# Performance work log

Measured on AMD Instinct MI355X. Metric: run time of the kernel, lower is better.

## Reference

```python
import jax, jax.numpy as jnp
import numpy as np

REP_DIM = 256
ATT_DIM = 256
AGRU_DIM = 256
BATCH = 64
MAX_FACTS = 512


def setup_inputs() -> dict:
    key = jax.random.key(0)
    ks = jax.random.split(key, 16)

    def lin(k, out_d, in_d):
        return jax.random.normal(k, (out_d, in_d), dtype=jnp.float32) / np.sqrt(in_d)

    inp = {
        "queries": jax.random.normal(ks[0], (BATCH, 1, REP_DIM), dtype=jnp.float32),
        "facts": jax.random.normal(ks[1], (BATCH, MAX_FACTS, REP_DIM), dtype=jnp.float32),
        "num_facts": jax.random.randint(ks[2], (BATCH,), 1, MAX_FACTS + 1, dtype=jnp.int32),
        "m_old": jax.random.normal(ks[3], (BATCH, 1, REP_DIM), dtype=jnp.float32),
        # attention MLP
        "W1_w": lin(ks[4], ATT_DIM, 4 * REP_DIM),
        "W1_b": jnp.zeros((ATT_DIM,), jnp.float32),
        "W2_w": lin(ks[5], 1, ATT_DIM),
        "W2_b": jnp.zeros((1,), jnp.float32),
        # attention GRU cell
        "Wr_w": lin(ks[6], AGRU_DIM, REP_DIM),
        "Ur_w": lin(ks[7], AGRU_DIM, AGRU_DIM),
        "Ur_b": jnp.zeros((AGRU_DIM,), jnp.float32),
        "Wg_w": lin(ks[8], AGRU_DIM, REP_DIM),
        "Ug_w": lin(ks[9], AGRU_DIM, AGRU_DIM),
        "Ug_b": jnp.zeros((AGRU_DIM,), jnp.float32),
        # output transform
        "Wt_w": lin(ks[10], REP_DIM, 2 * REP_DIM + AGRU_DIM),
        "Wt_b": jnp.zeros((REP_DIM,), jnp.float32),
    }
    return inp


def _forward(queries, facts, num_facts, m_old,
             W1_w, W1_b, W2_w, W2_b,
             Wr_w, Ur_w, Ur_b, Wg_w, Ug_w, Ug_b,
             Wt_w, Wt_b):
    B, T, D = facts.shape

    # ---- attention scores ----
    q = queries  # (B,1,D) broadcasts
    m = m_old
    z = jnp.concatenate(
        [facts * q, facts * m, jnp.abs(facts - q), jnp.abs(facts - m)], axis=2
    )  # (B,T,4D)
    Z = jnp.tanh(jnp.einsum("btf,af->bta", z, W1_w) + W1_b)
    Z = jnp.einsum("bta,oa->bto", Z, W2_w) + W2_b  # (B,T,1)
    mask = (jnp.arange(T)[None, :] < num_facts[:, None])[..., None]  # (B,T,1)
    Z = jnp.where(mask, Z, -jnp.inf)
    g = jax.nn.softmax(Z, axis=1)  # (B,T,1)

    # ---- attention GRU (sequential scan over facts) ----
    h0 = m_old[:, 0]  # (B,A)

    def step(h, xs):
        fact, g_t = xs  # (B,D), (B,1)
        r = jax.nn.sigmoid(fact @ Wr_w.T + h @ Ur_w.T + Ur_b)
        h_t = jnp.tanh(fact @ Wg_w.T + r * (h @ Ug_w.T + Ug_b))
        h_new = g_t * h_t + (1.0 - g_t) * h
        return h_new, h_new

    xs = (jnp.swapaxes(facts, 0, 1), jnp.swapaxes(g, 0, 1))  # (T,B,D),(T,B,1)
    _, states = jax.lax.scan(step, h0, xs)  # (T,B,A)
    c = jnp.take_along_axis(
        states, (num_facts - 1)[None, :, None].astype(jnp.int32), axis=0
    )[0]  # (B,A)

    # ---- next memory ----
    cat = jnp.concatenate([m_old[:, 0], c, queries[:, 0]], axis=1)
    m_new = jax.nn.relu(cat @ Wt_w.T + Wt_b)
    return m_new[:, None, :]  # (B,1,D)


def reference(queries, facts, num_facts, m_old,
              W1_w, W1_b, W2_w, W2_b,
              Wr_w, Ur_w, Ur_b, Wg_w, Ug_w, Ug_b,
              Wt_w, Wt_b):
    return _forward(queries, facts, num_facts, m_old,
                    W1_w, W1_b, W2_w, W2_b,
                    Wr_w, Ur_w, Ur_b, Wg_w, Ug_w, Ug_b,
                    Wt_w, Wt_b)
```

## Files before the change

### kernel.cpp

```cpp
#include <hip/hip_runtime.h>
#include <hip/hip_fp16.h>
#include <stdint.h>

#define B 64
#define T 512
#define D 256

typedef _Float16 f16;
typedef __attribute__((ext_vector_type(8))) _Float16 f16x8;
typedef __attribute__((ext_vector_type(4))) _Float16 f16x4;
typedef __attribute__((ext_vector_type(2))) _Float16 f16x2;
typedef __attribute__((ext_vector_type(4))) float f32x4;
typedef __attribute__((ext_vector_type(4))) unsigned int u32x4;

static __device__ __forceinline__ float dot2f(f16x2 a, f16x2 b, float c) {
  return __builtin_amdgcn_fdot2(a, b, c, false);
}
static __device__ __forceinline__ f16x2 as_h2(unsigned int u) {
  return __builtin_bit_cast(f16x2, u);
}

__global__ void k_convert(const float* __restrict__ W1, const float* __restrict__ Wr,
                          const float* __restrict__ Wg,
                          f16* __restrict__ W1h, f16* __restrict__ Wrh, f16* __restrict__ Wgh)
{
  const int64_t n1 = 256 * 1024, n2 = 65536, n3 = 65536;
  int64_t stride = (int64_t)gridDim.x * blockDim.x;
  for (int64_t i = (int64_t)blockIdx.x * blockDim.x + threadIdx.x; i < n1 + n2 + n3; i += stride) {
    if (i < n1)           W1h[i] = (f16)W1[i];
    else if (i < n1 + n2) Wrh[i - n1] = (f16)Wr[i - n1];
    else                  Wgh[i - n1 - n2] = (f16)Wg[i - n1 - n2];
  }
}

__global__ __launch_bounds__(256, 2) void k_attn(
    const float* __restrict__ facts, const float* __restrict__ queries,
    const float* __restrict__ m_old, const f16* __restrict__ W1h,
    const float* __restrict__ W1_b, const float* __restrict__ W2_w,
    const float* __restrict__ W2_b, float* __restrict__ Zlog)
{
  const int b = blockIdx.y;
  const int t0 = blockIdx.x * 32;
  const int tid = threadIdx.x;
  const int lane = tid & 63;
  const int wave = tid >> 6;
  const int lr = lane & 15;
  const int lg = lane >> 4;

  __shared__ float q_s[D], m_s[D];
  __shared__ __align__(16) char zbuf[32 * 2048];
  __shared__ float part[4][32];

  q_s[tid] = queries[b * D + tid];
  m_s[tid] = m_old[b * D + tid];
  __syncthreads();

  for (int e = tid; e < 32 * 128; e += 256) {
    int t = e >> 7;
    int j2 = e & 127;
    int j = j2 * 2;
    const float2 f2 = *(const float2*)(facts + ((int64_t)(b * T) + t0 + t) * D + j);
    float q0 = q_s[j], q1 = q_s[j + 1], mm0 = m_s[j], mm1 = m_s[j + 1];
    f16x2 z0; z0[0] = (f16)(f2.x * q0);        z0[1] = (f16)(f2.y * q1);
    f16x2 z1; z1[0] = (f16)(f2.x * mm0);       z1[1] = (f16)(f2.y * mm1);
    f16x2 z2; z2[0] = (f16)fabsf(f2.x - q0);   z2[1] = (f16)fabsf(f2.y - q1);
    f16x2 z3; z3[0] = (f16)fabsf(f2.x - mm0);  z3[1] = (f16)fabsf(f2.y - mm1);
    int xr = (t & 7) << 4;
    int base = t * 2048;
    *(f16x2*)(zbuf + ((base + (0 * 128 + j2) * 4) ^ xr)) = z0;
    *(f16x2*)(zbuf + ((base + (1 * 128 + j2) * 4) ^ xr)) = z1;
    *(f16x2*)(zbuf + ((base + (2 * 128 + j2) * 4) ^ xr)) = z2;
    *(f16x2*)(zbuf + ((base + (3 * 128 + j2) * 4) ^ xr)) = z3;
  }
  __syncthreads();

  const int n0 = wave * 64;
  f32x4 acc[2][4];
  #pragma unroll
  for (int i = 0; i < 2; ++i)
    #pragma unroll
    for (int j = 0; j < 4; ++j) acc[i][j] = (f32x4){0.f, 0.f, 0.f, 0.f};

  #pragma unroll 2
  for (int ks = 0; ks < 32; ++ks) {
    f16x8 af[2];
    #pragma unroll
    for (int mt = 0; mt < 2; ++mt) {
      int row = mt * 16 + lr;
      int byte = (row * 2048 + ks * 64 + lg * 16) ^ ((row & 7) << 4);
      af[mt] = *(const f16x8*)(zbuf + byte);
    }
    #pragma unroll
    for (int nt = 0; nt < 4; ++nt) {
      int a = n0 + nt * 16 + lr;
      f16x8 bf = *(const f16x8*)(W1h + (int64_t)a * 1024 + ks * 32 + lg * 8);
      acc[0][nt] = __builtin_amdgcn_mfma_f32_16x16x32_f16(af[0], bf, acc[0][nt], 0, 0, 0);
      acc[1][nt] = __builtin_amdgcn_mfma_f32_16x16x32_f16(af[1], bf, acc[1][nt], 0, 0, 0);
    }
  }

  float pr[2][4] = {{0.f, 0.f, 0.f, 0.f}, {0.f, 0.f, 0.f, 0.f}};
  #pragma unroll
  for (int nt = 0; nt < 4; ++nt) {
    int a = n0 + nt * 16 + lr;
    float b1 = W1_b[a];
    float w2 = W2_w[a];
    #pragma unroll
    for (int mt = 0; mt < 2; ++mt)
      #pragma unroll
      for (int r = 0; r < 4; ++r)
        pr[mt][r] += tanhf(acc[mt][nt][r] + b1) * w2;
  }
  #pragma unroll
  for (int mt = 0; mt < 2; ++mt)
    #pragma unroll
    for (int r = 0; r < 4; ++r) {
      float v = pr[mt][r];
      v += __shfl_xor(v, 1, 64);
      v += __shfl_xor(v, 2, 64);
      v += __shfl_xor(v, 4, 64);
      v += __shfl_xor(v, 8, 64);
      pr[mt][r] = v;
    }
  if ((lane & 15) == 0) {
    #pragma unroll
    for (int mt = 0; mt < 2; ++mt)
      #pragma unroll
      for (int r = 0; r < 4; ++r)
        part[wave][mt * 16 + lg * 4 + r] = pr[mt][r];
  }
  __syncthreads();
  if (tid < 32)
    Zlog[b * T + t0 + tid] = part[0][tid] + part[1][tid] + part[2][tid] + part[3][tid] + W2_b[0];
}

__global__ __launch_bounds__(256, 2) void k_factproj(
    const float* __restrict__ facts, const f16* __restrict__ Wrh, const f16* __restrict__ Wgh,
    const float* __restrict__ Ur_b, f16* __restrict__ Frh, f16* __restrict__ Fgh)
{
  const int b = blockIdx.y;
  const int t0 = blockIdx.x * 64;
  const int tid = threadIdx.x;
  const int lane = tid & 63;
  const int wave = tid >> 6;
  const int lr = lane & 15;
  const int lg = lane >> 4;

  __shared__ __align__(16) char albuf[64 * 512];

  for (int c = tid; c < 64 * 32; c += 256) {
    int row = c >> 5;
    int kc = c & 31;
    const float* src = facts + ((int64_t)(b * T) + t0 + row) * D + kc * 8;
    float4 x0 = *(const float4*)src;
    float4 x1 = *(const float4*)(src + 4);
    f16x8 v;
    v[0] = (f16)x0.x; v[1] = (f16)x0.y; v[2] = (f16)x0.z; v[3] = (f16)x0.w;
    v[4] = (f16)x1.x; v[5] = (f16)x1.y; v[6] = (f16)x1.z; v[7] = (f16)x1.w;
    int byte = (row * 512 + kc * 16) ^ ((row & 7) << 4);
    *(f16x8*)(albuf + byte) = v;
  }
  __syncthreads();

  f32x4 accr[16], accg[16];
  #pragma unroll
  for (int i = 0; i < 16; ++i) { accr[i] = (f32x4){0.f,0.f,0.f,0.f}; accg[i] = (f32x4){0.f,0.f,0.f,0.f}; }

  const int arow = wave * 16 + lr;
  #pragma unroll 2
  for (int ks = 0; ks < 8; ++ks) {
    int byte = (arow * 512 + ks * 64 + lg * 16) ^ ((arow & 7) << 4);
    f16x8 af = *(const f16x8*)(albuf + byte);
    #pragma unroll
    for (int nt = 0; nt < 16; ++nt) {
      int a = nt * 16 + lr;
      f16x8 br = *(const f16x8*)(Wrh + a * 256 + ks * 32 + lg * 8);
      f16x8 bg = *(const f16x8*)(Wgh + a * 256 + ks * 32 + lg * 8);
      accr[nt] = __builtin_amdgcn_mfma_f32_16x16x32_f16(af, br, accr[nt], 0, 0, 0);
      accg[nt] = __builtin_amdgcn_mfma_f32_16x16x32_f16(af, bg, accg[nt], 0, 0, 0);
    }
  }

  #pragma unroll
  for (int nt = 0; nt < 16; ++nt) {
    int col = nt * 16 + lr;
    float urb = Ur_b[col];
    #pragma unroll
    for (int r = 0; r < 4; ++r) {
      int t = t0 + wave * 16 + lg * 4 + r;
      int64_t off = ((int64_t)(b * T) + t) * D + col;
      Frh[off] = (f16)(accr[nt][r] + urb);
      Fgh[off] = (f16)(accg[nt][r]);
    }
  }
}

__global__ __launch_bounds__(256, 1) void k_scan_v6(
    const float* __restrict__ Zlog, const int* __restrict__ num_facts,
    const f16* __restrict__ Frh, const f16* __restrict__ Fgh,
    const float* __restrict__ Ur_w, const float* __restrict__ Ug_w,
    const float* __restrict__ Ug_b, const float* __restrict__ m_old,
    const float* __restrict__ queries, const float* __restrict__ Wt_w,
    const float* __restrict__ Wt_b, float* __restrict__ out)
{
  const int b = blockIdx.x;
  const int tid = threadIdx.x;
  const int lane = tid & 63;
  const int w = tid >> 6;
  const int q = lane >> 5;
  const int p = w * 32 + (lane & 31);
  const int nf = num_facts[b];

  __shared__ __align__(16) char hbuf[2][544];
  __shared__ float g_lds[512];
  __shared__ float redM[4], redS[4];
  __shared__ __align__(16) float cat_s[768];

  {
    float z0 = Zlog[b * 512 + tid];
    float z1 = Zlog[b * 512 + 256 + tid];
    float v0 = (tid < nf) ? z0 : -INFINITY;
    float v1 = (tid + 256 < nf) ? z1 : -INFINITY;
    float mx = fmaxf(v0, v1);
    #pragma unroll
    for (int s = 1; s < 64; s <<= 1) mx = fmaxf(mx, __shfl_xor(mx, s, 64));
    if (lane == 0) redM[w] = mx;
    __syncthreads();
    mx = fmaxf(fmaxf(redM[0], redM[1]), fmaxf(redM[2], redM[3]));
    float e0 = (tid < nf) ? __expf(v0 - mx) : 0.f;
    float e1 = (tid + 256 < nf) ? __expf(v1 - mx) : 0.f;
    float sum = e0 + e1;
    #pragma unroll
    for (int s = 1; s < 64; s <<= 1) sum += __shfl_xor(sum, s, 64);
    if (lane == 0) redS[w] = sum;
    __syncthreads();
    float inv = 1.f / (redS[0] + redS[1] + redS[2] + redS[3]);
    g_lds[tid] = e0 * inv;
    g_lds[256 + tid] = e1 * inv;
  }

  f16x2 wR[2][64], wG[2][64];
  #pragma unroll
  for (int j = 0; j < 2; ++j) {
    const float* ur = Ur_w + (int64_t)(2 * p + j) * 256 + q * 128;
    const float* ug = Ug_w + (int64_t)(2 * p + j) * 256 + q * 128;
    #pragma unroll
    for (int c = 0; c < 32; ++c) {
      float4 a = *(const float4*)(ur + c * 4);
      float4 g4 = *(const float4*)(ug + c * 4);
      f16x2 p0; p0[0] = (f16)a.x;  p0[1] = (f16)a.y;
      f16x2 p1; p1[0] = (f16)a.z;  p1[1] = (f16)a.w;
      f16x2 q0; q0[0] = (f16)g4.x; q0[1] = (f16)g4.y;
      f16x2 q1; q1[0] = (f16)g4.z; q1[1] = (f16)g4.w;
      wR[j][c * 2 + 0] = p0;
      wR[j][c * 2 + 1] = p1;
      wG[j][c * 2 + 0] = q0;
      wG[j][c * 2 + 1] = q1;
    }
  }

  float2 h2 = *(const float2*)(m_old + (int64_t)b * 256 + 2 * p);
  float h0 = h2.x, h1 = h2.y;
  float2 ub2 = *(const float2*)(Ug_b + 2 * p);

  const int waddr = 4 * p + (p >= 64 ? 16 : 0);
  if (q == 0) {
    f16x2 hp; hp[0] = (f16)h0; hp[1] = (f16)h1;
    *(f16x2*)(&hbuf[0][waddr]) = hp;
  }

  const f16* __restrict__ frp = Frh + (int64_t)(b * T) * D + 2 * p;
  const f16* __restrict__ fgp = Fgh + (int64_t)(b * T) * D + 2 * p;
  f16x2 frv = *(const f16x2*)frp;
  f16x2 fgv = *(const f16x2*)fgp;

  __syncthreads();

  for (int t = 0; t < nf; ++t) {
    const char* hb = hbuf[t & 1] + q * 272;
    u32x4 hv[4];
    #pragma unroll
    for (int c = 0; c < 4; ++c) hv[c] = *(const u32x4*)(hb + c * 16);
    u32x4 hw[4];
    #pragma unroll
    for (int c = 0; c < 4; ++c) hw[c] = *(const u32x4*)(hb + 64 + c * 16);
    u32x4 hx[4];
    #pragma unroll
    for (int c = 0; c < 4; ++c) hx[c] = *(const u32x4*)(hb + 128 + c * 16);
    u32x4 hy[4];
    #pragma unroll
    for (int c = 0; c < 4; ++c) hy[c] = *(const u32x4*)(hb + 192 + c * 16);

    f16x2 nfr = {}, nfg = {};
    if (t + 1 < nf) {
      nfr = *(const f16x2*)(frp + (int64_t)(t + 1) * D);
      nfg = *(const f16x2*)(fgp + (int64_t)(t + 1) * D);
    }
    float gt = g_lds[t];

    float aR0a = 0.f, aR0b = 0.f, aR1a = 0.f, aR1b = 0.f;
    float aG0a = 0.f, aG0b = 0.f, aG1a = 0.f, aG1b = 0.f;
    unsigned hu[64];
    #pragma unroll
    for (int c = 0; c < 4; ++c) {
      hu[c * 4 + 0]  = hv[c].x; hu[c * 4 + 1]  = hv[c].y; hu[c * 4 + 2]  = hv[c].z; hu[c * 4 + 3]  = hv[c].w;
      hu[16 + c * 4 + 0] = hw[c].x; hu[16 + c * 4 + 1] = hw[c].y; hu[16 + c * 4 + 2] = hw[c].z; hu[16 + c * 4 + 3] = hw[c].w;
      hu[32 + c * 4 + 0] = hx[c].x; hu[32 + c * 4 + 1] = hx[c].y; hu[32 + c * 4 + 2] = hx[c].z; hu[32 + c * 4 + 3] = hx[c].w;
      hu[48 + c * 4 + 0] = hy[c].x; hu[48 + c * 4 + 1] = hy[c].y; hu[48 + c * 4 + 2] = hy[c].z; hu[48 + c * 4 + 3] = hy[c].w;
    }
    #pragma unroll
    for (int i2 = 0; i2 < 32; ++i2) {
      f16x2 ha = as_h2(hu[i2 * 2]);
      f16x2 hbv = as_h2(hu[i2 * 2 + 1]);
      aR0a = dot2f(ha, wR[0][i2 * 2], aR0a);
      aR0b = dot2f(hbv, wR[0][i2 * 2 + 1], aR0b);
      aR1a = dot2f(ha, wR[1][i2 * 2], aR1a);
      aR1b = dot2f(hbv, wR[1][i2 * 2 + 1], aR1b);
      aG0a = dot2f(ha, wG[0][i2 * 2], aG0a);
      aG0b = dot2f(hbv, wG[0][i2 * 2 + 1], aG0b);
      aG1a = dot2f(ha, wG[1][i2 * 2], aG1a);
      aG1b = dot2f(hbv, wG[1][i2 * 2 + 1], aG1b);
    }
    float aR0 = aR0a + aR0b, aR1 = aR1a + aR1b;
    float aG0 = aG0a + aG0b, aG1 = aG1a + aG1b;
    aR0 += __shfl_xor(aR0, 32, 64);
    aR1 += __shfl_xor(aR1, 32, 64);
    aG0 += __shfl_xor(aG0, 32, 64);
    aG1 += __shfl_xor(aG1, 32, 64);

    {
      float fr0 = (float)frv[0], fr1 = (float)frv[1];
      float fg0 = (float)fgv[0], fg1 = (float)fgv[1];
      float rr0 = __builtin_amdgcn_rcpf(1.f + __expf(-(fr0 + aR0)));
      float rr1 = __builtin_amdgcn_rcpf(1.f + __expf(-(fr1 + aR1)));
      float y0 = fg0 + rr0 * (aG0 + ub2.x);
      float y1 = fg1 + rr1 * (aG1 + ub2.y);
      float ht0 = 1.f - 2.f * __builtin_amdgcn_rcpf(1.f + __expf(2.f * y0));
      float ht1 = 1.f - 2.f * __builtin_amdgcn_rcpf(1.f + __expf(2.f * y1));
      h0 = h0 + gt * (ht0 - h0);
      h1 = h1 + gt * (ht1 - h1);
    }
    if (q == 0) {
      f16x2 hp; hp[0] = (f16)h0; hp[1] = (f16)h1;
      *(f16x2*)(&hbuf[(t + 1) & 1][waddr]) = hp;
    }
    frv = nfr;
    fgv = nfg;
    __syncthreads();
  }

  cat_s[tid]       = m_old[(int64_t)b * 256 + tid];
  cat_s[512 + tid] = queries[(int64_t)b * 256 + tid];
  if (q == 0) {
    cat_s[256 + 2 * p]     = h0;
    cat_s[256 + 2 * p + 1] = h1;
  }
  __syncthreads();
  {
    const float* wrow = Wt_w + (int64_t)tid * 768;
    float acc = 0.f;
    #pragma unroll 8
    for (int k = 0; k < 768; k += 4) {
      float4 wv = *(const float4*)(wrow + k);
      float4 c4 = *(const float4*)(cat_s + k);
      acc += wv.x * c4.x + wv.y * c4.y + wv.z * c4.z + wv.w * c4.w;
    }
    out[(int64_t)b * 256 + tid] = fmaxf(acc + Wt_b[tid], 0.f);
  }
}

extern "C" void kernel_launch(void* const* d_in, const int* in_sizes, int n_in,
                              void* d_out, int out_size, void* d_ws, size_t ws_size,
                              hipStream_t stream)
{
  const float* queries   = (const float*)d_in[0];
  const float* facts     = (const float*)d_in[1];
  const int*   num_facts = (const int*)d_in[2];
  const float* m_old     = (const float*)d_in[3];
  const float* W1_w = (const float*)d_in[4];
  const float* W1_b = (const float*)d_in[5];
  const float* W2_w = (const float*)d_in[6];
  const float* W2_b = (const float*)d_in[7];
  const float* Wr_w = (const float*)d_in[8];
  const float* Ur_w = (const float*)d_in[9];
  const float* Ur_b = (const float*)d_in[10];
  const float* Wg_w = (const float*)d_in[11];
  const float* Ug_w = (const float*)d_in[12];
  const float* Ug_b = (const float*)d_in[13];
  const float* Wt_w = (const float*)d_in[14];
  const float* Wt_b = (const float*)d_in[15];
  float* out = (float*)d_out;

  char* p = (char*)d_ws;
  auto alloc = [&](size_t bytes) { char* r = p; p += (bytes + 255) & ~(size_t)255; return r; };
  f16*   W1h  = (f16*)alloc((size_t)256 * 1024 * 2);
  f16*   Wrh  = (f16*)alloc((size_t)65536 * 2);
  f16*   Wgh  = (f16*)alloc((size_t)65536 * 2);
  float* Zlog = (float*)alloc((size_t)B * T * 4);
  f16*   Frh  = (f16*)alloc((size_t)B * T * D * 2);
  f16*   Fgh  = (f16*)alloc((size_t)B * T * D * 2);

  k_convert<<<dim3(768), dim3(256), 0, stream>>>(W1_w, Wr_w, Wg_w, W1h, Wrh, Wgh);
  k_attn<<<dim3(16, 64), dim3(256), 0, stream>>>(facts, queries, m_old, W1h, W1_b, W2_w, W2_b, Zlog);
  k_factproj<<<dim3(8, 64), dim3(256), 0, stream>>>(facts, Wrh, Wgh, Ur_b, Frh, Fgh);
  k_scan_v6<<<dim3(64), dim3(256), 0, stream>>>(Zlog, num_facts, Frh, Fgh, Ur_w, Ug_w, Ug_b,
                                                m_old, queries, Wt_w, Wt_b, out);
}
```

Before: 811.1 us.

## Split GRU scan recurrence across 512 threads with 4-way K split and DPP reduce

The sequential scan kernel now runs with 512 threads per batch row. Each output pair is handled by 4 lanes that each own a quarter of the hidden dimension, so the per-thread recurrent dot-product chain is halved and the weight registers shrink. The partial sums are reduced with DPP quad swizzles instead of a cross-half shuffle, and the LDS layout of h is padded for the 4-way split. The cost is more waves taking part in each per-step block barrier and more LDS reads of h per step.

```diff
diff --git a/kernel.cpp b/kernel.cpp
--- a/kernel.cpp
+++ b/kernel.cpp
@@ -18,6 +18,14 @@
 }
 static __device__ __forceinline__ f16x2 as_h2(unsigned int u) {
   return __builtin_bit_cast(f16x2, u);
+}
+static __device__ __forceinline__ float dpp_add_xor1(float x) {
+  int s = __builtin_amdgcn_update_dpp(0, __builtin_bit_cast(int, x), 0xB1, 0xf, 0xf, true);
+  return x + __builtin_bit_cast(float, s);
+}
+static __device__ __forceinline__ float dpp_add_xor2(float x) {
+  int s = __builtin_amdgcn_update_dpp(0, __builtin_bit_cast(int, x), 0x4E, 0xf, 0xf, true);
+  return x + __builtin_bit_cast(float, s);
 }
 
 __global__ void k_convert(const float* __restrict__ W1, const float* __restrict__ Wr,
@@ -195,7 +203,7 @@
   }
 }
 
-__global__ __launch_bounds__(256, 1) void k_scan_v6(
+__global__ __launch_bounds__(512, 1) void k_scan_v7(
     const float* __restrict__ Zlog, const int* __restrict__ num_facts,
     const f16* __restrict__ Frh, const f16* __restrict__ Fgh,
     const float* __restrict__ Ur_w, const float* __restrict__ Ug_w,
@@ -207,45 +215,44 @@
   const int tid = threadIdx.x;
   const int lane = tid & 63;
   const int w = tid >> 6;
-  const int q = lane >> 5;
-  const int p = w * 32 + (lane & 31);
+  const int kq = lane & 3;
+  const int pi = w * 16 + (lane >> 2);
   const int nf = num_facts[b];
 
-  __shared__ __align__(16) char hbuf[2][544];
+  __shared__ __align__(16) char hbuf[2][576];
   __shared__ float g_lds[512];
-  __shared__ float redM[4], redS[4];
+  __shared__ float redM[8], redS[8];
   __shared__ __align__(16) float cat_s[768];
 
   {
-    float z0 = Zlog[b * 512 + tid];
-    float z1 = Zlog[b * 512 + 256 + tid];
-    float v0 = (tid < nf) ? z0 : -INFINITY;
-    float v1 = (tid + 256 < nf) ? z1 : -INFINITY;
-    float mx = fmaxf(v0, v1);
+    float z = Zlog[b * 512 + tid];
+    float v = (tid < nf) ? z : -INFINITY;
+    float mx = v;
     #pragma unroll
     for (int s = 1; s < 64; s <<= 1) mx = fmaxf(mx, __shfl_xor(mx, s, 64));
     if (lane == 0) redM[w] = mx;
     __syncthreads();
-    mx = fmaxf(fmaxf(redM[0], redM[1]), fmaxf(redM[2], redM[3]));
-    float e0 = (tid < nf) ? __expf(v0 - mx) : 0.f;
-    float e1 = (tid + 256 < nf) ? __expf(v1 - mx) : 0.f;
-    float sum = e0 + e1;
+    mx = redM[0];
+    #pragma unroll
+    for (int j = 1; j < 8; ++j) mx = fmaxf(mx, redM[j]);
+    float e = (tid < nf) ? __expf(v - mx) : 0.f;
+    float sum = e;
     #pragma unroll
     for (int s = 1; s < 64; s <<= 1) sum += __shfl_xor(sum, s, 64);
     if (lane == 0) redS[w] = sum;
     __syncthreads();
-    float inv = 1.f / (redS[0] + redS[1] + redS[2] + redS[3]);
-    g_lds[tid] = e0 * inv;
-    g_lds[256 + tid] = e1 * inv;
-  }
-
-  f16x2 wR[2][64], wG[2][64];
+    float inv = 1.f / (redS[0] + redS[1] + redS[2] + redS[3] +
+                       redS[4] + redS[5] + redS[6] + redS[7]);
+    g_lds[tid] = e * inv;
+  }
+
+  f16x2 wR[2][32], wG[2][32];
   #pragma unroll
   for (int j = 0; j < 2; ++j) {
-    const float* ur = Ur_w + (int64_t)(2 * p + j) * 256 + q * 128;
-    const float* ug = Ug_w + (int64_t)(2 * p + j) * 256 + q * 128;
-    #pragma unroll
-    for (int c = 0; c < 32; ++c) {
+    const float* ur = Ur_w + (int64_t)(2 * pi + j) * 256 + kq * 64;
+    const float* ug = Ug_w + (int64_t)(2 * pi + j) * 256 + kq * 64;
+    #pragma unroll
+    for (int c = 0; c < 16; ++c) {
       float4 a = *(const float4*)(ur + c * 4);
       float4 g4 = *(const float4*)(ug + c * 4);
       f16x2 p0; p0[0] = (f16)a.x;  p0[1] = (f16)a.y;
@@ -259,74 +266,66 @@
     }
   }
 
-  float2 h2 = *(const float2*)(m_old + (int64_t)b * 256 + 2 * p);
+  float2 h2 = *(const float2*)(m_old + (int64_t)b * 256 + 2 * pi);
   float h0 = h2.x, h1 = h2.y;
-  float2 ub2 = *(const float2*)(Ug_b + 2 * p);
-
-  const int waddr = 4 * p + (p >= 64 ? 16 : 0);
-  if (q == 0) {
+  float2 ub2 = *(const float2*)(Ug_b + 2 * pi);
+
+  const int hwaddr = ((2 * pi) >> 6) * 144 + ((2 * pi) & 63) * 2;
+  if (kq == 0) {
     f16x2 hp; hp[0] = (f16)h0; hp[1] = (f16)h1;
-    *(f16x2*)(&hbuf[0][waddr]) = hp;
-  }
-
-  const f16* __restrict__ frp = Frh + (int64_t)(b * T) * D + 2 * p;
-  const f16* __restrict__ fgp = Fgh + (int64_t)(b * T) * D + 2 * p;
+    *(f16x2*)(&hbuf[0][hwaddr]) = hp;
+  }
+
+  const f16* __restrict__ frp = Frh + (int64_t)(b * T) * D + 2 * pi;
+  const f16* __restrict__ fgp = Fgh + (int64_t)(b * T) * D + 2 * pi;
   f16x2 frv = *(const f16x2*)frp;
   f16x2 fgv = *(const f16x2*)fgp;
 
   __syncthreads();
 
   for (int t = 0; t < nf; ++t) {
-    const char* hb = hbuf[t & 1] + q * 272;
-    u32x4 hv[4];
-    #pragma unroll
-    for (int c = 0; c < 4; ++c) hv[c] = *(const u32x4*)(hb + c * 16);
-    u32x4 hw[4];
-    #pragma unroll
-    for (int c = 0; c < 4; ++c) hw[c] = *(const u32x4*)(hb + 64 + c * 16);
-    u32x4 hx[4];
-    #pragma unroll
-    for (int c = 0; c < 4; ++c) hx[c] = *(const u32x4*)(hb + 128 + c * 16);
-    u32x4 hy[4];
-    #pragma unroll
-    for (int c = 0; c < 4; ++c) hy[c] = *(const u32x4*)(hb + 192 + c * 16);
-
+    const char* hb = hbuf[t & 1] + kq * 144;
+    u32x4 hv[8];
+    #pragma unroll
+    for (int c = 0; c < 8; ++c) hv[c] = *(const u32x4*)(hb + c * 16);
+
+    float gt = g_lds[t];
     f16x2 nfr = {}, nfg = {};
     if (t + 1 < nf) {
       nfr = *(const f16x2*)(frp + (int64_t)(t + 1) * D);
       nfg = *(const f16x2*)(fgp + (int64_t)(t + 1) * D);
     }
-    float gt = g_lds[t];
 
     float aR0a = 0.f, aR0b = 0.f, aR1a = 0.f, aR1b = 0.f;
     float aG0a = 0.f, aG0b = 0.f, aG1a = 0.f, aG1b = 0.f;
-    unsigned hu[64];
-    #pragma unroll
-    for (int c = 0; c < 4; ++c) {
-      hu[c * 4 + 0]  = hv[c].x; hu[c * 4 + 1]  = hv[c].y; hu[c * 4 + 2]  = hv[c].z; hu[c * 4 + 3]  = hv[c].w;
-      hu[16 + c * 4 + 0] = hw[c].x; hu[16 + c * 4 + 1] = hw[c].y; hu[16 + c * 4 + 2] = hw[c].z; hu[16 + c * 4 + 3] = hw[c].w;
-      hu[32 + c * 4 + 0] = hx[c].x; hu[32 + c * 4 + 1] = hx[c].y; hu[32 + c * 4 + 2] = hx[c].z; hu[32 + c * 4 + 3] = hx[c].w;
-      hu[48 + c * 4 + 0] = hy[c].x; hu[48 + c * 4 + 1] = hy[c].y; hu[48 + c * 4 + 2] = hy[c].z; hu[48 + c * 4 + 3] = hy[c].w;
-    }
-    #pragma unroll
-    for (int i2 = 0; i2 < 32; ++i2) {
-      f16x2 ha = as_h2(hu[i2 * 2]);
-      f16x2 hbv = as_h2(hu[i2 * 2 + 1]);
-      aR0a = dot2f(ha, wR[0][i2 * 2], aR0a);
-      aR0b = dot2f(hbv, wR[0][i2 * 2 + 1], aR0b);
-      aR1a = dot2f(ha, wR[1][i2 * 2], aR1a);
-      aR1b = dot2f(hbv, wR[1][i2 * 2 + 1], aR1b);
-      aG0a = dot2f(ha, wG[0][i2 * 2], aG0a);
-      aG0b = dot2f(hbv, wG[0][i2 * 2 + 1], aG0b);
-      aG1a = dot2f(ha, wG[1][i2 * 2], aG1a);
-      aG1b = dot2f(hbv, wG[1][i2 * 2 + 1], aG1b);
+    #pragma unroll
+    for (int c = 0; c < 8; ++c) {
+      f16x2 x0 = as_h2(hv[c].x), x1 = as_h2(hv[c].y);
+      f16x2 x2 = as_h2(hv[c].z), x3 = as_h2(hv[c].w);
+      int i0 = c * 4;
+      aR0a = dot2f(x0, wR[0][i0 + 0], aR0a);
+      aR0b = dot2f(x1, wR[0][i0 + 1], aR0b);
+      aR0a = dot2f(x2, wR[0][i0 + 2], aR0a);
+      aR0b = dot2f(x3, wR[0][i0 + 3], aR0b);
+      aR1a = dot2f(x0, wR[1][i0 + 0], aR1a);
+      aR1b = dot2f(x1, wR[1][i0 + 1], aR1b);
+      aR1a = dot2f(x2, wR[1][i0 + 2], aR1a);
+      aR1b = dot2f(x3, wR[1][i0 + 3], aR1b);
+      aG0a = dot2f(x0, wG[0][i0 + 0], aG0a);
+      aG0b = dot2f(x1, wG[0][i0 + 1], aG0b);
+      aG0a = dot2f(x2, wG[0][i0 + 2], aG0a);
+      aG0b = dot2f(x3, wG[0][i0 + 3], aG0b);
+      aG1a = dot2f(x0, wG[1][i0 + 0], aG1a);
+      aG1b = dot2f(x1, wG[1][i0 + 1], aG1b);
+      aG1a = dot2f(x2, wG[1][i0 + 2], aG1a);
+      aG1b = dot2f(x3, wG[1][i0 + 3], aG1b);
     }
     float aR0 = aR0a + aR0b, aR1 = aR1a + aR1b;
     float aG0 = aG0a + aG0b, aG1 = aG1a + aG1b;
-    aR0 += __shfl_xor(aR0, 32, 64);
-    aR1 += __shfl_xor(aR1, 32, 64);
-    aG0 += __shfl_xor(aG0, 32, 64);
-    aG1 += __shfl_xor(aG1, 32, 64);
+    aR0 = dpp_add_xor2(dpp_add_xor1(aR0));
+    aR1 = dpp_add_xor2(dpp_add_xor1(aR1));
+    aG0 = dpp_add_xor2(dpp_add_xor1(aG0));
+    aG1 = dpp_add_xor2(dpp_add_xor1(aG1));
 
     {
       float fr0 = (float)frv[0], fr1 = (float)frv[1];
@@ -340,23 +339,23 @@
       h0 = h0 + gt * (ht0 - h0);
       h1 = h1 + gt * (ht1 - h1);
     }
-    if (q == 0) {
+    if (kq == 0) {
       f16x2 hp; hp[0] = (f16)h0; hp[1] = (f16)h1;
-      *(f16x2*)(&hbuf[(t + 1) & 1][waddr]) = hp;
+      *(f16x2*)(&hbuf[(t + 1) & 1][hwaddr]) = hp;
     }
     frv = nfr;
     fgv = nfg;
     __syncthreads();
   }
 
-  cat_s[tid]       = m_old[(int64_t)b * 256 + tid];
-  cat_s[512 + tid] = queries[(int64_t)b * 256 + tid];
-  if (q == 0) {
-    cat_s[256 + 2 * p]     = h0;
-    cat_s[256 + 2 * p + 1] = h1;
-  }
-  __syncthreads();
-  {
+  if (tid < 256) cat_s[tid] = m_old[(int64_t)b * 256 + tid];
+  else           cat_s[256 + tid] = queries[(int64_t)b * 256 + (tid - 256)];
+  if (kq == 0) {
+    cat_s[256 + 2 * pi]     = h0;
+    cat_s[256 + 2 * pi + 1] = h1;
+  }
+  __syncthreads();
+  if (tid < 256) {
     const float* wrow = Wt_w + (int64_t)tid * 768;
     float acc = 0.f;
     #pragma unroll 8
@@ -403,6 +402,6 @@
   k_convert<<<dim3(768), dim3(256), 0, stream>>>(W1_w, Wr_w, Wg_w, W1h, Wrh, Wgh);
   k_attn<<<dim3(16, 64), dim3(256), 0, stream>>>(facts, queries, m_old, W1h, W1_b, W2_w, W2_b, Zlog);
   k_factproj<<<dim3(8, 64), dim3(256), 0, stream>>>(facts, Wrh, Wgh, Ur_b, Frh, Fgh);
-  k_scan_v6<<<dim3(64), dim3(256), 0, stream>>>(Zlog, num_facts, Frh, Fgh, Ur_w, Ug_w, Ug_b,
+  k_scan_v7<<<dim3(64), dim3(512), 0, stream>>>(Zlog, num_facts, Frh, Fgh, Ur_w, Ug_w, Ug_b,
                                                 m_old, queries, Wt_w, Wt_b, out);
 }
```

New measurement: 709.2 us. -12.6%, faster.
